# Optimization experiments

Hardware: AMD Instinct MI355X
Metric: run time of the kernel (lower is better)

The kernel has to match this reference:

```python
import jax, jax.numpy as jnp
import numpy as np

BIG = 1e8  # sentinel 'infinite' squared distance (sqrt(BIG) >> max real distance)


def _edt_sq(feat):
    """Exact squared Euclidean distance transform to the nearest True pixel.
    feat: (H, W) bool. Separable 1-D min-plus envelopes (exact, matches
    scipy.ndimage.distance_transform_edt with unit sampling)."""
    H, W = feat.shape
    f = jnp.where(feat, 0.0, BIG).astype(jnp.float32)
    iw = jnp.arange(W, dtype=jnp.float32)
    sqw = (iw[:, None] - iw[None, :]) ** 2                      # (Wx, Wy)
    d1 = jnp.min(f[:, None, :] + sqw[None, :, :], axis=-1)      # (H, W) row pass
    ih = jnp.arange(H, dtype=jnp.float32)
    sqh = (ih[:, None] - ih[None, :]) ** 2                      # (Hx, Hy)
    d2 = jnp.min(d1[None, :, :] + sqh[:, :, None], axis=1)      # (H, W) col pass
    return d2


def _phi_one(mask):
    # pos: distance to nearest mask==1 pixel (scipy edt of 1-mask)
    # neg: distance to nearest mask==0 pixel (scipy edt of mask)
    pos = jnp.sqrt(_edt_sq(mask))
    neg = jnp.sqrt(_edt_sq(~mask))
    s = mask.sum()
    return jnp.where(s == 0, pos,
                     jnp.where(s == mask.size, -neg, pos - neg + 1.0))


def _boundary_loss(logits, targets):
    B, C, H, W = logits.shape
    probs = jax.nn.softmax(logits, axis=1)
    # one-hot scatter: (B,H,W) -> (B,C,H,W)
    oh = jax.nn.one_hot(targets, C, dtype=jnp.float32).transpose(0, 3, 1, 2)
    masks = (oh > 0.5).reshape(B * C, H, W)
    phi = jax.lax.map(_phi_one, masks).reshape(B, C, H, W)
    phi = jax.lax.stop_gradient(phi)  # torch computes phi under no_grad
    return jnp.mean(probs * phi)


def setup_inputs() -> dict:
    key = jax.random.key(0)
    k1, k2 = jax.random.split(key)
    B, C, H, W = 8, 4, 384, 384
    logits = jax.random.normal(k1, (B, C, H, W), dtype=jnp.float32)
    targets = jax.random.randint(k2, (B, H, W), 0, C, dtype=jnp.int32)
    return {"logits": logits, "targets": targets}


def reference(logits, targets):
    return _boundary_loss(logits, targets)
```

## Files before the change

kernel.cpp:

```cpp
#include <hip/hip_runtime.h>


#define BB 8
#define CC 4
#define HH 384
#define WW 384
#define HW (HH * WW)
#define NTOT 4718592.0f

__global__ __launch_bounds__(384) void k_rowedt(const int* __restrict__ targets,
                                                unsigned short* __restrict__ edt16,
                                                float* __restrict__ out) {
    const int blk = blockIdx.x;
    const int b = blk / HH;
    const int i = blk - b * HH;
    const int j = threadIdx.x;
    const int wv = j >> 6, ln = j & 63;

    __shared__ unsigned long long msk[CC][6];
    const int tj = targets[((size_t)b * HH + i) * WW + j];

    #pragma unroll
    for (int c = 0; c < CC; ++c) {
        const unsigned long long m = __ballot(tj == c);
        if (ln == 0) msk[c][wv] = m;
    }
    __syncthreads();

    #pragma unroll
    for (int c = 0; c < CC; ++c) {
        const unsigned long long w = msk[c][wv];
        int dR = 0xFFFF;
        const unsigned long long x = (ln == 63) ? 0ull : (w >> (ln + 1));
        if (x) {
            dR = __builtin_ctzll(x) + 1;
        } else {
            for (int k = wv + 1; k < 6; ++k) {
                const unsigned long long wk = msk[c][k];
                if (wk) { dR = 64 * k + __builtin_ctzll(wk) - j; break; }
            }
        }
        int dL = 0xFFFF;
        const unsigned long long y = (ln == 0) ? 0ull : (w << (64 - ln));
        if (y) {
            dL = __builtin_clzll(y) + 1;
        } else {
            for (int k = wv - 1; k >= 0; --k) {
                const unsigned long long wk = msk[c][k];
                if (wk) { dL = j - (64 * k + 63 - __builtin_clzll(wk)); break; }
            }
        }
        const int fd = (tj == c) ? 0 : (dR < dL ? dR : dL);
        edt16[(size_t)(b * CC + c) * HW + (size_t)i * WW + j] = (unsigned short)fd;
    }

    if (blk == 0 && j == 0) out[0] = 0.0f;
}

__device__ __forceinline__ float minplus_col(const float* __restrict__ sqc,
                                             int i, int col) {
    float best = sqc[i * 13 + col];
    float dd = 1.0f, odd = 3.0f;
    int lo = i, hi = i;
    while (dd < best) {
        lo = (lo > 0) ? lo - 1 : 0;
        hi = (hi < HH - 1) ? hi + 1 : HH - 1;
        best = fminf(best, fminf(sqc[lo * 13 + col] + dd, sqc[hi * 13 + col] + dd));
        dd += odd; odd += 2.0f;
    }
    return best;
}

__global__ __launch_bounds__(384) void k_fused(const unsigned short* __restrict__ edt16,
                                               const float* __restrict__ logits,
                                               float* __restrict__ out) {
    const int blk = blockIdx.x;
    const int b = blk >> 5;
    const int tile = blk & 31;
    const int j0 = tile * 12;
    const int col = threadIdx.x % 12;
    const int rg  = threadIdx.x / 12;

    __shared__ float sq[2][HH][13];

    #pragma unroll
    for (int cc = 0; cc < 2; ++cc) {
        #pragma unroll
        for (int k = 0; k < 12; ++k) {
            const int i = rg + 32 * k;
            const unsigned int v =
                edt16[(size_t)(b * CC + cc) * HW + (size_t)i * WW + j0 + col];
            sq[cc][i][col] = (float)(v * v);
        }
    }
    __syncthreads();

    float r01[2][12];
    #pragma unroll
    for (int k = 0; k < 12; ++k) {
        const int i = rg + 32 * k;
        r01[0][k] = sqrtf(minplus_col(&sq[0][0][0], i, col));
        r01[1][k] = sqrtf(minplus_col(&sq[1][0][0], i, col));
    }
    __syncthreads();

    #pragma unroll
    for (int cc = 0; cc < 2; ++cc) {
        #pragma unroll
        for (int k = 0; k < 12; ++k) {
            const int i = rg + 32 * k;
            const unsigned int v =
                edt16[(size_t)(b * CC + 2 + cc) * HW + (size_t)i * WW + j0 + col];
            sq[cc][i][col] = (float)(v * v);
        }
    }
    __syncthreads();

    float acc = 0.0f;
    #pragma unroll
    for (int k = 0; k < 12; ++k) {
        const int i = rg + 32 * k;
        const float r0 = r01[0][k];
        const float r1 = r01[1][k];
        const float r2 = sqrtf(minplus_col(&sq[0][0][0], i, col));
        const float r3 = sqrtf(minplus_col(&sq[1][0][0], i, col));

        const float p0 = r0 - fminf(r1, fminf(r2, r3)) + 1.0f;
        const float p1 = r1 - fminf(r0, fminf(r2, r3)) + 1.0f;
        const float p2 = r2 - fminf(r0, fminf(r1, r3)) + 1.0f;
        const float p3 = r3 - fminf(r0, fminf(r1, r2)) + 1.0f;

        const size_t po = (size_t)i * WW + j0 + col;
        const size_t pb = (size_t)b * CC * HW;
        const float l0 = logits[pb + 0 * HW + po];
        const float l1 = logits[pb + 1 * HW + po];
        const float l2 = logits[pb + 2 * HW + po];
        const float l3 = logits[pb + 3 * HW + po];
        const float m  = fmaxf(fmaxf(l0, l1), fmaxf(l2, l3));
        const float e0 = __expf(l0 - m), e1 = __expf(l1 - m);
        const float e2 = __expf(l2 - m), e3 = __expf(l3 - m);
        const float inv = 1.0f / (e0 + e1 + e2 + e3);
        acc += inv * (e0 * p0 + e1 * p1 + e2 * p2 + e3 * p3);
    }

    #pragma unroll
    for (int off = 32; off > 0; off >>= 1) acc += __shfl_down(acc, off, 64);
    __shared__ float wsum[6];
    const int wid = threadIdx.x >> 6, ln = threadIdx.x & 63;
    if (ln == 0) wsum[wid] = acc;
    __syncthreads();
    if (threadIdx.x == 0) {
        float tot = 0.0f;
        #pragma unroll
        for (int w = 0; w < 6; ++w) tot += wsum[w];
        atomicAdd(out, tot * (1.0f / NTOT));
    }
}

extern "C" void kernel_launch(void* const* d_in, const int* in_sizes, int n_in,
                              void* d_out, int out_size, void* d_ws, size_t ws_size,
                              hipStream_t stream) {
    const float* logits  = (const float*)d_in[0];
    const int*   targets = (const int*)d_in[1];
    float* out = (float*)d_out;
    unsigned short* edt16 = (unsigned short*)d_ws;

    hipLaunchKernelGGL(k_rowedt, dim3(BB * HH), dim3(WW), 0, stream, targets, edt16, out);
    hipLaunchKernelGGL(k_fused,  dim3(BB * 32), dim3(384), 0, stream, edt16, logits, out);
}
```

Measured before the change: 102.1 us.

## Split column pass over row quarters and fuse paired min-plus searches

The column-pass kernel now launches four blocks per 16-column tile, each block handling one quarter of the rows. This raises the grid from 256 blocks to 768 for more occupancy, with each thread doing 4 rows instead of 12. The two channels' min-plus expanding searches now share one loop that runs until both have converged, which cuts loop overhead but lets divergence follow the slower channel. Every block still loads the full column strips into shared memory, so global and LDS load traffic grows about fourfold.

```diff
diff --git a/kernel.cpp b/kernel.cpp
--- a/kernel.cpp
+++ b/kernel.cpp
@@ -57,37 +57,25 @@
     if (blk == 0 && j == 0) out[0] = 0.0f;
 }
 
-__device__ __forceinline__ float minplus_col(const float* __restrict__ sqc,
-                                             int i, int col) {
-    float best = sqc[i * 13 + col];
-    float dd = 1.0f, odd = 3.0f;
-    int lo = i, hi = i;
-    while (dd < best) {
-        lo = (lo > 0) ? lo - 1 : 0;
-        hi = (hi < HH - 1) ? hi + 1 : HH - 1;
-        best = fminf(best, fminf(sqc[lo * 13 + col] + dd, sqc[hi * 13 + col] + dd));
-        dd += odd; odd += 2.0f;
-    }
-    return best;
-}
-
 __global__ __launch_bounds__(384) void k_fused(const unsigned short* __restrict__ edt16,
                                                const float* __restrict__ logits,
                                                float* __restrict__ out) {
     const int blk = blockIdx.x;
-    const int b = blk >> 5;
-    const int tile = blk & 31;
-    const int j0 = tile * 12;
-    const int col = threadIdx.x % 12;
-    const int rg  = threadIdx.x / 12;
+    const int q = blk & 3;
+    const int bt = blk >> 2;
+    const int b = bt / 24;
+    const int tile = bt - b * 24;
+    const int j0 = tile * 16;
+    const int col = threadIdx.x & 15;
+    const int rg  = threadIdx.x >> 4;
 
-    __shared__ float sq[2][HH][13];
+    __shared__ float sq[2][HH][17];
 
     #pragma unroll
     for (int cc = 0; cc < 2; ++cc) {
         #pragma unroll
-        for (int k = 0; k < 12; ++k) {
-            const int i = rg + 32 * k;
+        for (int k = 0; k < 16; ++k) {
+            const int i = rg + 24 * k;
             const unsigned int v =
                 edt16[(size_t)(b * CC + cc) * HW + (size_t)i * WW + j0 + col];
             sq[cc][i][col] = (float)(v * v);
@@ -95,20 +83,31 @@
     }
     __syncthreads();
 
-    float r01[2][12];
+    float r01[2][4];
     #pragma unroll
-    for (int k = 0; k < 12; ++k) {
-        const int i = rg + 32 * k;
-        r01[0][k] = sqrtf(minplus_col(&sq[0][0][0], i, col));
-        r01[1][k] = sqrtf(minplus_col(&sq[1][0][0], i, col));
+    for (int k = 0; k < 4; ++k) {
+        const int i = q * 96 + rg + 24 * k;
+        float b0 = sq[0][i][col];
+        float b1 = sq[1][i][col];
+        float dd = 1.0f, odd = 3.0f;
+        int lo = i, hi = i;
+        while (dd < fmaxf(b0, b1)) {
+            lo = (lo > 0) ? lo - 1 : 0;
+            hi = (hi < HH - 1) ? hi + 1 : HH - 1;
+            b0 = fminf(b0, fminf(sq[0][lo][col], sq[0][hi][col]) + dd);
+            b1 = fminf(b1, fminf(sq[1][lo][col], sq[1][hi][col]) + dd);
+            dd += odd; odd += 2.0f;
+        }
+        r01[0][k] = sqrtf(b0);
+        r01[1][k] = sqrtf(b1);
     }
     __syncthreads();
 
     #pragma unroll
     for (int cc = 0; cc < 2; ++cc) {
         #pragma unroll
-        for (int k = 0; k < 12; ++k) {
-            const int i = rg + 32 * k;
+        for (int k = 0; k < 16; ++k) {
+            const int i = rg + 24 * k;
             const unsigned int v =
                 edt16[(size_t)(b * CC + 2 + cc) * HW + (size_t)i * WW + j0 + col];
             sq[cc][i][col] = (float)(v * v);
@@ -118,12 +117,23 @@
 
     float acc = 0.0f;
     #pragma unroll
-    for (int k = 0; k < 12; ++k) {
-        const int i = rg + 32 * k;
+    for (int k = 0; k < 4; ++k) {
+        const int i = q * 96 + rg + 24 * k;
+        float b2 = sq[0][i][col];
+        float b3 = sq[1][i][col];
+        float dd = 1.0f, odd = 3.0f;
+        int lo = i, hi = i;
+        while (dd < fmaxf(b2, b3)) {
+            lo = (lo > 0) ? lo - 1 : 0;
+            hi = (hi < HH - 1) ? hi + 1 : HH - 1;
+            b2 = fminf(b2, fminf(sq[0][lo][col], sq[0][hi][col]) + dd);
+            b3 = fminf(b3, fminf(sq[1][lo][col], sq[1][hi][col]) + dd);
+            dd += odd; odd += 2.0f;
+        }
         const float r0 = r01[0][k];
         const float r1 = r01[1][k];
-        const float r2 = sqrtf(minplus_col(&sq[0][0][0], i, col));
-        const float r3 = sqrtf(minplus_col(&sq[1][0][0], i, col));
+        const float r2 = sqrtf(b2);
+        const float r3 = sqrtf(b3);
 
         const float p0 = r0 - fminf(r1, fminf(r2, r3)) + 1.0f;
         const float p1 = r1 - fminf(r0, fminf(r2, r3)) + 1.0f;
@@ -166,5 +176,5 @@
     unsigned short* edt16 = (unsigned short*)d_ws;
 
     hipLaunchKernelGGL(k_rowedt, dim3(BB * HH), dim3(WW), 0, stream, targets, edt16, out);
-    hipLaunchKernelGGL(k_fused,  dim3(BB * 32), dim3(384), 0, stream, edt16, logits, out);
+    hipLaunchKernelGGL(k_fused,  dim3(BB * 24 * 4), dim3(384), 0, stream, edt16, logits, out);
 }
```

New measurement: 98.37 us, median of 2. 1.04x faster.
